# Optimization experiments

Hardware: AMD Instinct MI355X
Metric: run time of the kernel (lower is better)

The kernel has to match this reference:

```python
import jax, jax.numpy as jnp
import numpy as np
import math

M = 512          # num_bin_x
NB = 512         # num_bin_y
NUM_NODES = 2_000_000
K = 4            # max bins a node can overlap per dim (size <= 2.5 bins)
SQRT2 = math.sqrt(2.0)


def setup_inputs() -> dict:
    key = jax.random.key(0)
    k1, k2 = jax.random.split(key)
    node_pos = jax.random.uniform(k1, (NUM_NODES, 2), jnp.float32, 0.05, 0.95)
    # node sizes between 0.5 and 2.5 bins (normalized layout units)
    node_size = jax.random.uniform(k2, (NUM_NODES, 2), jnp.float32) * (2.0 / M) + (0.5 / M)
    return {
        "node_pos": node_pos,
        "node_size": node_size,
        "node_weight": jnp.ones((NUM_NODES,), jnp.float32),
        "expand_ratio": jnp.ones((NUM_NODES,), jnp.float32),
        "unit_len": jnp.array([1.0 / M, 1.0 / NB], jnp.float32),
        "init_density_map": jnp.zeros((M, NB), jnp.float32),
        "num_bin_x": M,
        "num_bin_y": NB,
    }


def pre_normalize(node_pos, node_size, node_weight, expand_ratio, unit_len, mx, ny):
    # density_map_cuda.pre_normalize: expand tiny nodes to sqrt(2)*unit_len,
    # rescale weight to preserve area, convert rects to bin coordinates.
    ux, uy = unit_len[0], unit_len[1]
    w, h = node_size[:, 0], node_size[:, 1]
    new_w = jnp.maximum(w, SQRT2 * ux)
    new_h = jnp.maximum(h, SQRT2 * uy)
    weight = node_weight * expand_ratio * (w * h) / (new_w * new_h)
    xl = jnp.clip((node_pos[:, 0] - 0.5 * new_w) / ux, 0.0, mx)
    xh = jnp.clip((node_pos[:, 0] + 0.5 * new_w) / ux, 0.0, mx)
    yl = jnp.clip((node_pos[:, 1] - 0.5 * new_h) / uy, 0.0, ny)
    yh = jnp.clip((node_pos[:, 1] + 0.5 * new_h) / uy, 0.0, ny)
    return jnp.stack([xl, xh, yl, yh, weight], axis=1)  # [N, 5]


def scatter_density(info, mx, ny):
    # density_map_cuda.forward: overlap-area scatter-add of node rects into bins.
    xl, xh, yl, yh, w = info[:, 0], info[:, 1], info[:, 2], info[:, 3], info[:, 4]
    bx0 = jnp.floor(xl).astype(jnp.int32)
    by0 = jnp.floor(yl).astype(jnp.int32)
    dm = jnp.zeros((mx, ny), jnp.float32)
    for dx in range(K):
        ix = bx0 + dx
        fx = ix.astype(jnp.float32)
        ox = jnp.clip(jnp.minimum(xh, fx + 1.0) - jnp.maximum(xl, fx), 0.0)
        ixc = jnp.clip(ix, 0, mx - 1)
        for dy in range(K):
            iy = by0 + dy
            fy = iy.astype(jnp.float32)
            oy = jnp.clip(jnp.minimum(yh, fy + 1.0) - jnp.maximum(yl, fy), 0.0)
            iyc = jnp.clip(iy, 0, ny - 1)
            dm = dm.at[ixc, iyc].add(w * ox * oy)
    return dm


def make_transforms(n):
    k = jnp.arange(n, dtype=jnp.float32)[:, None]
    m = jnp.arange(n, dtype=jnp.float32)[None, :]
    ang = jnp.pi * k * (2.0 * m + 1.0) / (2.0 * n)
    C = jnp.cos(ang)  # [freq, space]
    S = jnp.sin(ang)
    w = jnp.where(jnp.arange(n) == 0, 1.0, 2.0).astype(jnp.float32)
    return C, S, w


def spectral_solve(dm, unit_len, mx, ny):
    # fft_scale construction from __init__
    wj = (jnp.arange(mx, dtype=jnp.float32) * (2.0 * jnp.pi / mx))[:, None]
    wk = (jnp.arange(ny, dtype=jnp.float32) * (2.0 * jnp.pi / ny))[None, :]
    wk = wk * (unit_len[0] / unit_len[1])  # scale_w_k=True
    wsq = wj ** 2 + wk ** 2
    wsq = wsq.at[0, 0].set(1.0)
    pscale = (1.0 / wsq).at[0, 0].set(0.0)
    fx_scale = wj * pscale * 0.5
    fy_scale = wk * pscale * 0.5

    Cx, Sx, wx = make_transforms(mx)
    Cy, Sy, wy = make_transforms(ny)
    # dct2: coeff[u,v] = (1/(M*N)) * sum_{m,n} dm[m,n] cos(pi u(2m+1)/2M) cos(pi v(2n+1)/2N)
    coeff = (Cx @ dm @ Cy.T) / (mx * ny)
    ICx = (wx[:, None] * Cx)  # weighted inverse cosine basis [freq, space]
    ICy = (wy[:, None] * Cy)
    ISx = (wx[:, None] * Sx)
    ISy = (wy[:, None] * Sy)
    potential = ICx.T @ (coeff * pscale) @ ICy          # idct2
    force_x = ISx.T @ (coeff * fx_scale) @ ICy          # idxst_idct
    force_y = ICx.T @ (coeff * fy_scale) @ ISy          # idct_idxst
    return potential, force_x, force_y


def reference(node_pos, node_size, node_weight, expand_ratio, unit_len,
              init_density_map, num_bin_x, num_bin_y):
    info = pre_normalize(node_pos, node_size, node_weight, expand_ratio,
                         unit_len, num_bin_x, num_bin_y)
    density_map = init_density_map + scatter_density(info, num_bin_x, num_bin_y)
    potential, _, _ = spectral_solve(density_map, unit_len, num_bin_x, num_bin_y)
    energy = jnp.sum(potential * density_map)
    return energy
```

## Files before the change

kernel.cpp:

```cpp
#include <hip/hip_runtime.h>
#include <math.h>

#define MX 512
#define NY 512
#define TWO_PI 6.283185307179586f

#define TSHIFT 6
#define NT 64
#define LDIM 68
#define SLAB (LDIM * LDIM)
#define SLAB4 (SLAB / 4)
#define NPB 2048
#define KPT 8
#define CAP 40960
#define SPTMAX 32
#define RPARTS 19
#define QSCALE 26214.0f
#define QINV (1.0f / 26214.0f)

typedef __attribute__((ext_vector_type(8))) short short8;
typedef __attribute__((ext_vector_type(4))) float float4_t;
typedef __attribute__((ext_vector_type(4))) unsigned short ushort4_t;

__device__ __forceinline__ unsigned short f2bf(float x) {
    union { float f; unsigned u; } v; v.f = x;
    unsigned r = v.u + 0x7fffu + ((v.u >> 16) & 1u);
    return (unsigned short)(r >> 16);
}
__device__ __forceinline__ float bf2f(unsigned short h) {
    union { float f; unsigned u; } v; v.u = ((unsigned)h) << 16;
    return v.f;
}

__device__ __forceinline__ void node_bounds(float2 p, float2 s, float ux, float uy,
                                            float& xl, float& xh, float& yl, float& yh,
                                            float& nw, float& nh) {
    const float SQ2 = 1.41421356237309515f;
    nw = fmaxf(s.x, SQ2 * ux);
    nh = fmaxf(s.y, SQ2 * uy);
    xl = fminf(fmaxf((p.x - 0.5f * nw) / ux, 0.0f), (float)MX);
    xh = fminf(fmaxf((p.x + 0.5f * nw) / ux, 0.0f), (float)MX);
    yl = fminf(fmaxf((p.y - 0.5f * nh) / uy, 0.0f), (float)NY);
    yh = fminf(fmaxf((p.y + 0.5f * nh) / uy, 0.0f), (float)NY);
}

__global__ void gen_cos_kernel(unsigned short* __restrict__ Ch,
                               unsigned short* __restrict__ Cl,
                               unsigned int* __restrict__ base,
                               unsigned int* __restrict__ cursor,
                               float* __restrict__ out, int cap_mode) {
    int idx = blockIdx.x * blockDim.x + threadIdx.x;
    if (idx == 0) *out = 0.0f;
    if (cap_mode && idx <= NT) {
        base[idx] = (unsigned int)idx * CAP;
        if (idx < NT) cursor[idx] = (unsigned int)idx * CAP;
    }
    int a = idx >> 9;
    int j = idx & 511;
    float x = cospif((float)(a * (2 * j + 1)) * (1.0f / 1024.0f));
    unsigned short hi = f2bf(x);
    Ch[idx] = hi;
    Cl[idx] = f2bf(x - bf2f(hi));
}

__global__ __launch_bounds__(256)
void count_kernel(const float2* __restrict__ pos, const float2* __restrict__ size,
                  const float* __restrict__ unit_len,
                  unsigned int* __restrict__ cnt, int n) {
    __shared__ unsigned int h[NT];
    if (threadIdx.x < NT) h[threadIdx.x] = 0;
    __syncthreads();
    float ux = unit_len[0], uy = unit_len[1];
    int start = blockIdx.x * NPB;
    int end = min(start + NPB, n);
#pragma unroll
    for (int k = 0; k < KPT; k++) {
        int i = start + k * 256 + (int)threadIdx.x;
        if (i < end) {
            float xl, xh, yl, yh, nw, nh;
            node_bounds(pos[i], size[i], ux, uy, xl, xh, yl, yh, nw, nh);
            int bx0 = min((int)floorf(xl), MX - 1);
            int by0 = min((int)floorf(yl), NY - 1);
            atomicAdd(&h[((bx0 >> TSHIFT) << 3) | (by0 >> TSHIFT)], 1u);
        }
    }
    __syncthreads();
    if (threadIdx.x < NT) {
        unsigned int c = h[threadIdx.x];
        if (c) atomicAdd(&cnt[threadIdx.x], c);
    }
}

__global__ void scan_kernel(const unsigned int* __restrict__ cnt,
                            unsigned int* __restrict__ base,
                            unsigned int* __restrict__ cursor) {
    if (threadIdx.x == 0 && blockIdx.x == 0) {
        unsigned int ex = 0;
        for (int t = 0; t < NT; t++) {
            base[t] = ex;
            cursor[t] = ex;
            ex += cnt[t];
        }
        base[NT] = ex;
    }
}

__global__ __launch_bounds__(256)
void place_kernel(const float2* __restrict__ pos, const float2* __restrict__ size,
                  const float* __restrict__ nwt, const float* __restrict__ er,
                  const float* __restrict__ unit_len,
                  const unsigned int* __restrict__ base,
                  unsigned int* __restrict__ cursor,
                  float4* __restrict__ pb, int n) {
    __shared__ unsigned int h[NT];
    __shared__ unsigned int lb[NT + 1];
    __shared__ unsigned int bb[NT];
    __shared__ float4 buf[NPB];
    __shared__ unsigned char til[NPB];
    if (threadIdx.x < NT) h[threadIdx.x] = 0;
    __syncthreads();
    float ux = unit_len[0], uy = unit_len[1];
    int start = blockIdx.x * NPB;
    int end = min(start + NPB, n);

    float cxl[KPT], cyl[KPT], cw[KPT];
    unsigned int cq[KPT], pk[KPT];
#pragma unroll
    for (int k = 0; k < KPT; k++) {
        int i = start + k * 256 + (int)threadIdx.x;
        if (i < end) {
            float2 p = pos[i], s = size[i];
            float xl, xh, yl, yh, nw, nh;
            node_bounds(p, s, ux, uy, xl, xh, yl, yh, nw, nh);
            cxl[k] = xl; cyl[k] = yl;
            cw[k] = nwt[i] * er[i] * (s.x * s.y) / (nw * nh);
            unsigned qx = (unsigned)((xh - xl) * QSCALE + 0.5f);
            unsigned qy = (unsigned)((yh - yl) * QSCALE + 0.5f);
            if (qx > 65535u) qx = 65535u;
            if (qy > 65535u) qy = 65535u;
            cq[k] = qx | (qy << 16);
            int bx0 = min((int)floorf(xl), MX - 1);
            int by0 = min((int)floorf(yl), NY - 1);
            unsigned int t = ((bx0 >> TSHIFT) << 3) | (by0 >> TSHIFT);
            pk[k] = (t << 11) | atomicAdd(&h[t], 1u);
        }
    }
    __syncthreads();
    if (threadIdx.x == 0) {
        unsigned int ex = 0;
        for (int t = 0; t < NT; t++) { lb[t] = ex; ex += h[t]; }
        lb[NT] = ex;
    }
    if (threadIdx.x < NT) {
        unsigned int c = h[threadIdx.x];
        bb[threadIdx.x] = c ? atomicAdd(&cursor[threadIdx.x], c) : 0u;
    }
    __syncthreads();
#pragma unroll
    for (int k = 0; k < KPT; k++) {
        int i = start + k * 256 + (int)threadIdx.x;
        if (i < end) {
            unsigned int t = pk[k] >> 11;
            unsigned int slot = lb[t] + (pk[k] & 2047u);
            buf[slot] = make_float4(cxl[k], cyl[k], cw[k], __uint_as_float(cq[k]));
            til[slot] = (unsigned char)t;
        }
    }
    __syncthreads();
    unsigned int total = lb[NT];
    for (unsigned int j = threadIdx.x; j < total; j += 256) {
        unsigned int t = til[j];
        unsigned int dst = bb[t] + (j - lb[t]);
        if (dst < base[t + 1]) pb[dst] = buf[j];
    }
}

__device__ __forceinline__ void accum_one(float4 v, float* acc, int tbx, int tby) {
    float xl = v.x, yl = v.y, w = v.z;
    unsigned q = __float_as_uint(v.w);
    float xh = xl + (float)(q & 0xffffu) * QINV;
    float yh = yl + (float)(q >> 16) * QINV;
    int bx0 = min((int)floorf(xl), MX - 1);
    int by0 = min((int)floorf(yl), NY - 1);
    float oxs[4], oys[4];
    int rb[4], lys[4];
#pragma unroll
    for (int d = 0; d < 4; d++) {
        int ix = bx0 + d;
        float fx = (float)ix;
        oxs[d] = fmaxf(fminf(xh, fx + 1.0f) - fmaxf(xl, fx), 0.0f);
        rb[d] = (min(ix, MX - 1) - tbx) * LDIM;
        int iy = by0 + d;
        float fy = (float)iy;
        oys[d] = fmaxf(fminf(yh, fy + 1.0f) - fmaxf(yl, fy), 0.0f);
        lys[d] = min(iy, NY - 1) - tby;
    }
#pragma unroll
    for (int dx = 0; dx < 4; dx++) {
        if (oxs[dx] == 0.0f) continue;
        float wox = w * oxs[dx];
#pragma unroll
        for (int dy = 0; dy < 4; dy++) {
            float vv = wox * oys[dy];
            if (vv != 0.0f) atomicAdd(&acc[rb[dx] + lys[dy]], vv);
        }
    }
}

__global__ __launch_bounds__(256)
void accum_kernel(const float4* __restrict__ pb,
                  const unsigned int* __restrict__ base,
                  const unsigned int* __restrict__ cursor,
                  float* __restrict__ slab, int spt) {
    __shared__ float acc[SLAB];
    int t = blockIdx.x / spt;
    int s = blockIdx.x - t * spt;
    int tbx = (t >> 3) << TSHIFT;
    int tby = (t & 7) << TSHIFT;
    for (int e = threadIdx.x; e < SLAB4; e += 256)
        ((float4*)acc)[e] = make_float4(0.f, 0.f, 0.f, 0.f);
    __syncthreads();

    unsigned int b0 = base[t];
    unsigned int c = min(cursor[t] - b0, base[t + 1] - b0);
    unsigned int chunk = (c + spt - 1) / spt;
    unsigned int ks = s * chunk;
    unsigned int ke = min(c, ks + chunk);

    unsigned int k = ks + threadIdx.x;
    float4 cur = make_float4(0.f, 0.f, 0.f, 0.f);
    bool have = (k < ke);
    if (have) cur = pb[b0 + k];
    while (have) {
        unsigned int k2 = k + 256;
        bool have2 = (k2 < ke);
        float4 nxt = make_float4(0.f, 0.f, 0.f, 0.f);
        if (have2) nxt = pb[b0 + k2];
        accum_one(cur, acc, tbx, tby);
        cur = nxt; k = k2; have = have2;
    }
    __syncthreads();

    float4* dst = (float4*)(slab + (size_t)blockIdx.x * SLAB);
    for (int e = threadIdx.x; e < SLAB4; e += 256)
        dst[e] = ((float4*)acc)[e];
}

__global__ __launch_bounds__(256)
void reduce_slabs_kernel(const float* __restrict__ slab,
                         float* __restrict__ tacc, int spt) {
    int t = blockIdx.x / RPARTS;
    int part = blockIdx.x - t * RPARTS;
    int e = part * 256 + (int)threadIdx.x;
    if (e < SLAB) {
        const float* s0 = slab + (size_t)t * spt * SLAB + e;
        float sum = 0.0f;
        for (int s = 0; s < spt; s++) sum += s0[(size_t)s * SLAB];
        tacc[(size_t)t * SLAB + e] = sum;
    }
}

__global__ __launch_bounds__(256)
void combine_kernel(const float* __restrict__ tacc,
                    const float* __restrict__ init_dm,
                    unsigned short* __restrict__ dmh,
                    unsigned short* __restrict__ dml) {
    int v = blockIdx.x * blockDim.x + threadIdx.x;
    int gx = v >> 7;
    int g4 = v & 127;
    int gy = g4 << 2;
    int rx = gx & 63, ry = gy & 63;
    int tx0 = gx >> TSHIFT, ty0 = gy >> TSHIFT;

    float4 sum = ((const float4*)init_dm)[v];
#pragma unroll
    for (int ax = 0; ax < 2; ax++) {
        int tx = tx0 - ax;
        if (tx < 0 || (ax == 1 && rx > 3)) continue;
        int lx = rx + (ax << TSHIFT);
#pragma unroll
        for (int ay = 0; ay < 2; ay++) {
            int ty = ty0 - ay;
            if (ty < 0 || (ay == 1 && ry > 0)) continue;
            int ly = ry + (ay << TSHIFT);
            float4 sv = *(const float4*)(tacc
                + (size_t)((tx << 3) | ty) * SLAB + lx * LDIM + ly);
            sum.x += sv.x; sum.y += sv.y; sum.z += sv.z; sum.w += sv.w;
        }
    }
    ushort4_t hi, lo;
    float sv[4] = {sum.x, sum.y, sum.z, sum.w};
#pragma unroll
    for (int r = 0; r < 4; r++) {
        unsigned short h = f2bf(sv[r]);
        hi[r] = h;
        lo[r] = f2bf(sv[r] - bf2f(h));
    }
    int idx = (gx << 9) | gy;
    *(ushort4_t*)(dmh + idx) = hi;
    *(ushort4_t*)(dml + idx) = lo;
}

__global__ __launch_bounds__(256)
void dct1_mfma_kernel(const unsigned short* __restrict__ dmh,
                      const unsigned short* __restrict__ dml,
                      const unsigned short* __restrict__ Ch,
                      const unsigned short* __restrict__ Cl,
                      unsigned short* __restrict__ UhT,
                      unsigned short* __restrict__ UlT) {
    __shared__ float part[3][64][4];
    int lane = threadIdx.x & 63;
    int wv = threadIdx.x >> 6;
    int tile = blockIdx.x;
    int jt = (tile >> 5) * 16;
    int bt = (tile & 31) * 16;
    int m = lane & 15, q = lane >> 4;
    float4_t acc = {0.f, 0.f, 0.f, 0.f};
    const unsigned short* ah_row = dmh + (jt + m) * 512;
    const unsigned short* al_row = dml + (jt + m) * 512;
    const unsigned short* bh_row = Ch + (bt + m) * 512;
    const unsigned short* bl_row = Cl + (bt + m) * 512;
    int kbase = wv * 128;
#pragma unroll
    for (int kk = 0; kk < 128; kk += 32) {
        int off = kbase + kk + q * 8;
        short8 ah = *(const short8*)(ah_row + off);
        short8 al = *(const short8*)(al_row + off);
        short8 bh = *(const short8*)(bh_row + off);
        short8 bl = *(const short8*)(bl_row + off);
        acc = __builtin_amdgcn_mfma_f32_16x16x32_bf16(ah, bh, acc, 0, 0, 0);
        acc = __builtin_amdgcn_mfma_f32_16x16x32_bf16(ah, bl, acc, 0, 0, 0);
        acc = __builtin_amdgcn_mfma_f32_16x16x32_bf16(al, bh, acc, 0, 0, 0);
    }
    if (wv > 0) {
#pragma unroll
        for (int r = 0; r < 4; r++) part[wv - 1][lane][r] = acc[r];
    }
    __syncthreads();
    if (wv == 0) {
#pragma unroll
        for (int r = 0; r < 4; r++) {
            float v = acc[r] + part[0][lane][r] + part[1][lane][r] + part[2][lane][r];
            unsigned short hi = f2bf(v);
            int addr = (bt + m) * 512 + jt + q * 4 + r;
            UhT[addr] = hi;
            UlT[addr] = f2bf(v - bf2f(hi));
        }
    }
}

__global__ __launch_bounds__(256)
void dct2_mfma_kernel(const unsigned short* __restrict__ Ch,
                      const unsigned short* __restrict__ Cl,
                      const unsigned short* __restrict__ UhT,
                      const unsigned short* __restrict__ UlT,
                      const float* __restrict__ unit_len,
                      float* __restrict__ out) {
    __shared__ float part[3][64][4];
    int lane = threadIdx.x & 63;
    int wv = threadIdx.x >> 6;
    int tile = blockIdx.x;
    int at = (tile >> 5) * 16;
    int bt = (tile & 31) * 16;
    int m = lane & 15, q = lane >> 4;
    float4_t acc = {0.f, 0.f, 0.f, 0.f};
    const unsigned short* ah_row = Ch + (at + m) * 512;
    const unsigned short* al_row = Cl + (at + m) * 512;
    const unsigned short* bh_row = UhT + (bt + m) * 512;
    const unsigned short* bl_row = UlT + (bt + m) * 512;
    int kbase = wv * 128;
#pragma unroll
    for (int kk = 0; kk < 128; kk += 32) {
        int off = kbase + kk + q * 8;
        short8 ah = *(const short8*)(ah_row + off);
        short8 al = *(const short8*)(al_row + off);
        short8 bh = *(const short8*)(bh_row + off);
        short8 bl = *(const short8*)(bl_row + off);
        acc = __builtin_amdgcn_mfma_f32_16x16x32_bf16(ah, bh, acc, 0, 0, 0);
        acc = __builtin_amdgcn_mfma_f32_16x16x32_bf16(ah, bl, acc, 0, 0, 0);
        acc = __builtin_amdgcn_mfma_f32_16x16x32_bf16(al, bh, acc, 0, 0, 0);
    }
    if (wv > 0) {
#pragma unroll
        for (int r = 0; r < 4; r++) part[wv - 1][lane][r] = acc[r];
    }
    __syncthreads();
    if (wv == 0) {
        float ratio = unit_len[0] / unit_len[1];
        int b = bt + m;
        float wkb = (float)b * (TWO_PI / (float)NY) * ratio;
        float wyb = (b == 0) ? 1.0f : 2.0f;
        float e = 0.0f;
#pragma unroll
        for (int r = 0; r < 4; r++) {
            float t = acc[r] + part[0][lane][r] + part[1][lane][r] + part[2][lane][r];
            int a = at + q * 4 + r;
            float wja = (float)a * (TWO_PI / (float)MX);
            float wsq = wja * wja + wkb * wkb;
            float ps = (a == 0 && b == 0) ? 0.0f : (1.0f / wsq);
            float wxa = (a == 0) ? 1.0f : 2.0f;
            e += wxa * wyb * ps * t * t;
        }
#pragma unroll
        for (int off = 32; off > 0; off >>= 1) e += __shfl_down(e, off, 64);
        if (lane == 0)
            atomicAdd(out, e * (1.0f / ((float)MX * (float)NY)));
    }
}

__global__ __launch_bounds__(256)
void scatter_kernel(const float2* __restrict__ pos, const float2* __restrict__ size,
                    const float* __restrict__ nwt, const float* __restrict__ er,
                    const float* __restrict__ unit_len,
                    float* __restrict__ dm, int n) {
    int i = blockIdx.x * blockDim.x + threadIdx.x;
    if (i >= n) return;
    float ux = unit_len[0], uy = unit_len[1];
    float2 p = pos[i], s = size[i];
    float xl, xh, yl, yh, nw, nh;
    node_bounds(p, s, ux, uy, xl, xh, yl, yh, nw, nh);
    float w = nwt[i] * er[i] * (s.x * s.y) / (nw * nh);
    int bx0 = (int)floorf(xl);
    int by0 = (int)floorf(yl);
#pragma unroll
    for (int dx = 0; dx < 4; dx++) {
        int ix = bx0 + dx;
        float fx = (float)ix;
        float ox = fmaxf(fminf(xh, fx + 1.0f) - fmaxf(xl, fx), 0.0f);
        if (ox == 0.0f) continue;
        int rowoff = min(max(ix, 0), MX - 1) * NY;
        float wox = w * ox;
#pragma unroll
        for (int dy = 0; dy < 4; dy++) {
            int iy = by0 + dy;
            float fy = (float)iy;
            float oy = fmaxf(fminf(yh, fy + 1.0f) - fmaxf(yl, fy), 0.0f);
            float vv = wox * oy;
            if (vv != 0.0f) atomicAdd(&dm[rowoff + min(max(iy, 0), NY - 1)], vv);
        }
    }
}

__global__ void cvt_dm_kernel(const float* __restrict__ dm,
                              unsigned short* __restrict__ dmh,
                              unsigned short* __restrict__ dml) {
    int idx = blockIdx.x * blockDim.x + threadIdx.x;
    float x = dm[idx];
    unsigned short hi = f2bf(x);
    dmh[idx] = hi;
    dml[idx] = f2bf(x - bf2f(hi));
}

extern "C" void kernel_launch(void* const* d_in, const int* in_sizes, int n_in,
                              void* d_out, int out_size, void* d_ws, size_t ws_size,
                              hipStream_t stream) {
    const float2* node_pos  = (const float2*)d_in[0];
    const float2* node_size = (const float2*)d_in[1];
    const float*  node_wt   = (const float*)d_in[2];
    const float*  exp_ratio = (const float*)d_in[3];
    const float*  unit_len  = (const float*)d_in[4];
    const float*  init_dm   = (const float*)d_in[5];
    float* out = (float*)d_out;
    int n = in_sizes[2];

    char* wsb = (char*)d_ws;
    size_t off = 0;
    auto alloc = [&](size_t bytes) { void* p = wsb + off; off = (off + bytes + 255) & ~(size_t)255; return p; };
    unsigned short* Ch   = (unsigned short*)alloc((size_t)MX * NY * 2);
    unsigned short* Cl   = (unsigned short*)alloc((size_t)MX * NY * 2);
    unsigned short* dmh  = (unsigned short*)alloc((size_t)MX * NY * 2);
    unsigned short* dml  = (unsigned short*)alloc((size_t)MX * NY * 2);
    unsigned short* UhT  = (unsigned short*)alloc((size_t)MX * NY * 2);
    unsigned short* UlT  = (unsigned short*)alloc((size_t)MX * NY * 2);
    float*          dm     = (float*)alloc((size_t)MX * NY * sizeof(float));
    unsigned int*   cnt    = (unsigned int*)alloc(NT * sizeof(unsigned int));
    unsigned int*   tbase  = (unsigned int*)alloc((NT + 1) * sizeof(unsigned int));
    unsigned int*   cursor = (unsigned int*)alloc(NT * sizeof(unsigned int));
    float*          tacc   = (float*)alloc((size_t)NT * SLAB * sizeof(float));
    size_t off_common = off;
    size_t per_spt = (size_t)NT * SLAB * sizeof(float);

    float4* pbF = (float4*)alloc((size_t)NT * CAP * sizeof(float4));
    int sptF = 0;
    float* slbF = nullptr;
    if (off <= ws_size) {
        sptF = (int)((ws_size - off) / per_spt);
        if (sptF > SPTMAX) sptF = SPTMAX;
        if (sptF >= 4) slbF = (float*)alloc((size_t)NT * sptF * SLAB * sizeof(float));
    }
    bool tierFast = (slbF != nullptr);

    off = off_common;
    float4* pbE = (float4*)alloc((size_t)n * sizeof(float4));
    int sptE = 0;
    float* slbE = nullptr;
    if (off <= ws_size) {
        sptE = (int)((ws_size - off) / per_spt);
        if (sptE > SPTMAX) sptE = SPTMAX;
        if (sptE >= 1) slbE = (float*)alloc((size_t)NT * sptE * SLAB * sizeof(float));
    }
    bool tierExact = (slbE != nullptr);

    gen_cos_kernel<<<(MX * NY) / 256, 256, 0, stream>>>(Ch, Cl, tbase, cursor,
                                                        out, tierFast ? 1 : 0);

    if (tierFast || tierExact) {
        float4* pb  = tierFast ? pbF : pbE;
        float*  slb = tierFast ? slbF : slbE;
        int     spt = tierFast ? sptF : sptE;
        int nblk = (n + NPB - 1) / NPB;
        if (!tierFast) {
            hipMemsetAsync(cnt, 0, NT * sizeof(unsigned int), stream);
            count_kernel<<<nblk, 256, 0, stream>>>(node_pos, node_size, unit_len, cnt, n);
            scan_kernel<<<1, 64, 0, stream>>>(cnt, tbase, cursor);
        }
        place_kernel<<<nblk, 256, 0, stream>>>(
            node_pos, node_size, node_wt, exp_ratio, unit_len, tbase, cursor, pb, n);
        accum_kernel<<<NT * spt, 256, 0, stream>>>(pb, tbase, cursor, slb, spt);
        reduce_slabs_kernel<<<NT * RPARTS, 256, 0, stream>>>(slb, tacc, spt);
        combine_kernel<<<256, 256, 0, stream>>>(tacc, init_dm, dmh, dml);
    } else {
        hipMemcpyAsync(dm, init_dm, (size_t)MX * NY * sizeof(float),
                       hipMemcpyDeviceToDevice, stream);
        scatter_kernel<<<(n + 255) / 256, 256, 0, stream>>>(
            node_pos, node_size, node_wt, exp_ratio, unit_len, dm, n);
        cvt_dm_kernel<<<(MX * NY) / 256, 256, 0, stream>>>(dm, dmh, dml);
    }

    dct1_mfma_kernel<<<1024, 256, 0, stream>>>(dmh, dml, Ch, Cl, UhT, UlT);
    dct2_mfma_kernel<<<1024, 256, 0, stream>>>(Ch, Cl, UhT, UlT, unit_len, out);
}
```

Before: 248.1 us.

## Fuse cosine gen, slab reduce, combine and both DCT passes into cooperative kernel

Merges cosine-table generation, slab reduction, density combine and the two MFMA DCT passes into one cooperative kernel that uses grid-wide syncs between stages. The fast tier also switches to fixed per-tile offsets (t*CAP) with a memset of the cursors, which removes base-array lookups. This cuts four kernel launches and their inter-kernel gaps. In exchange it relies on all 1024 blocks being co-resident and pays the cost of grid.sync barriers.

```diff
diff --git a/kernel.cpp b/kernel.cpp
--- a/kernel.cpp
+++ b/kernel.cpp
@@ -1,5 +1,8 @@
 #include <hip/hip_runtime.h>
+#include <hip/hip_cooperative_groups.h>
 #include <math.h>
+
+namespace cg = cooperative_groups;
 
 #define MX 512
 #define NY 512
@@ -14,7 +17,6 @@
 #define KPT 8
 #define CAP 40960
 #define SPTMAX 32
-#define RPARTS 19
 #define QSCALE 26214.0f
 #define QINV (1.0f / 26214.0f)
 
@@ -44,25 +46,6 @@
     yh = fminf(fmaxf((p.y + 0.5f * nh) / uy, 0.0f), (float)NY);
 }
 
-__global__ void gen_cos_kernel(unsigned short* __restrict__ Ch,
-                               unsigned short* __restrict__ Cl,
-                               unsigned int* __restrict__ base,
-                               unsigned int* __restrict__ cursor,
-                               float* __restrict__ out, int cap_mode) {
-    int idx = blockIdx.x * blockDim.x + threadIdx.x;
-    if (idx == 0) *out = 0.0f;
-    if (cap_mode && idx <= NT) {
-        base[idx] = (unsigned int)idx * CAP;
-        if (idx < NT) cursor[idx] = (unsigned int)idx * CAP;
-    }
-    int a = idx >> 9;
-    int j = idx & 511;
-    float x = cospif((float)(a * (2 * j + 1)) * (1.0f / 1024.0f));
-    unsigned short hi = f2bf(x);
-    Ch[idx] = hi;
-    Cl[idx] = f2bf(x - bf2f(hi));
-}
-
 __global__ __launch_bounds__(256)
 void count_kernel(const float2* __restrict__ pos, const float2* __restrict__ size,
                   const float* __restrict__ unit_len,
@@ -109,7 +92,7 @@
 void place_kernel(const float2* __restrict__ pos, const float2* __restrict__ size,
                   const float* __restrict__ nwt, const float* __restrict__ er,
                   const float* __restrict__ unit_len,
-                  const unsigned int* __restrict__ base,
+                  const unsigned int* __restrict__ basep,
                   unsigned int* __restrict__ cursor,
                   float4* __restrict__ pb, int n) {
     __shared__ unsigned int h[NT];
@@ -168,10 +151,18 @@
     }
     __syncthreads();
     unsigned int total = lb[NT];
-    for (unsigned int j = threadIdx.x; j < total; j += 256) {
-        unsigned int t = til[j];
-        unsigned int dst = bb[t] + (j - lb[t]);
-        if (dst < base[t + 1]) pb[dst] = buf[j];
+    if (basep) {
+        for (unsigned int j = threadIdx.x; j < total; j += 256) {
+            unsigned int t = til[j];
+            unsigned int dst = bb[t] + (j - lb[t]);
+            if (dst < basep[t + 1]) pb[dst] = buf[j];
+        }
+    } else {
+        for (unsigned int j = threadIdx.x; j < total; j += 256) {
+            unsigned int t = til[j];
+            unsigned int lofs = bb[t] + (j - lb[t]);
+            if (lofs < CAP) pb[(size_t)t * CAP + lofs] = buf[j];
+        }
     }
 }
 
@@ -209,7 +200,7 @@
 
 __global__ __launch_bounds__(256)
 void accum_kernel(const float4* __restrict__ pb,
-                  const unsigned int* __restrict__ base,
+                  const unsigned int* __restrict__ basep,
                   const unsigned int* __restrict__ cursor,
                   float* __restrict__ slab, int spt) {
     __shared__ float acc[SLAB];
@@ -221,8 +212,14 @@
         ((float4*)acc)[e] = make_float4(0.f, 0.f, 0.f, 0.f);
     __syncthreads();
 
-    unsigned int b0 = base[t];
-    unsigned int c = min(cursor[t] - b0, base[t + 1] - b0);
+    unsigned int b0g, c;
+    if (basep) {
+        b0g = basep[t];
+        c = min(cursor[t] - b0g, basep[t + 1] - b0g);
+    } else {
+        b0g = (unsigned int)t * CAP;
+        c = min(cursor[t], (unsigned int)CAP);
+    }
     unsigned int chunk = (c + spt - 1) / spt;
     unsigned int ks = s * chunk;
     unsigned int ke = min(c, ks + chunk);
@@ -230,12 +227,12 @@
     unsigned int k = ks + threadIdx.x;
     float4 cur = make_float4(0.f, 0.f, 0.f, 0.f);
     bool have = (k < ke);
-    if (have) cur = pb[b0 + k];
+    if (have) cur = pb[b0g + k];
     while (have) {
         unsigned int k2 = k + 256;
         bool have2 = (k2 < ke);
         float4 nxt = make_float4(0.f, 0.f, 0.f, 0.f);
-        if (have2) nxt = pb[b0 + k2];
+        if (have2) nxt = pb[b0g + k2];
         accum_one(cur, acc, tbx, tby);
         cur = nxt; k = k2; have = have2;
     }
@@ -246,165 +243,164 @@
         dst[e] = ((float4*)acc)[e];
 }
 
-__global__ __launch_bounds__(256)
-void reduce_slabs_kernel(const float* __restrict__ slab,
-                         float* __restrict__ tacc, int spt) {
-    int t = blockIdx.x / RPARTS;
-    int part = blockIdx.x - t * RPARTS;
-    int e = part * 256 + (int)threadIdx.x;
-    if (e < SLAB) {
-        const float* s0 = slab + (size_t)t * spt * SLAB + e;
-        float sum = 0.0f;
-        for (int s = 0; s < spt; s++) sum += s0[(size_t)s * SLAB];
-        tacc[(size_t)t * SLAB + e] = sum;
-    }
-}
-
-__global__ __launch_bounds__(256)
-void combine_kernel(const float* __restrict__ tacc,
-                    const float* __restrict__ init_dm,
-                    unsigned short* __restrict__ dmh,
-                    unsigned short* __restrict__ dml) {
-    int v = blockIdx.x * blockDim.x + threadIdx.x;
-    int gx = v >> 7;
-    int g4 = v & 127;
-    int gy = g4 << 2;
-    int rx = gx & 63, ry = gy & 63;
-    int tx0 = gx >> TSHIFT, ty0 = gy >> TSHIFT;
-
-    float4 sum = ((const float4*)init_dm)[v];
-#pragma unroll
-    for (int ax = 0; ax < 2; ax++) {
-        int tx = tx0 - ax;
-        if (tx < 0 || (ax == 1 && rx > 3)) continue;
-        int lx = rx + (ax << TSHIFT);
-#pragma unroll
-        for (int ay = 0; ay < 2; ay++) {
-            int ty = ty0 - ay;
-            if (ty < 0 || (ay == 1 && ry > 0)) continue;
-            int ly = ry + (ay << TSHIFT);
-            float4 sv = *(const float4*)(tacc
-                + (size_t)((tx << 3) | ty) * SLAB + lx * LDIM + ly);
-            sum.x += sv.x; sum.y += sv.y; sum.z += sv.z; sum.w += sv.w;
-        }
-    }
-    ushort4_t hi, lo;
-    float sv[4] = {sum.x, sum.y, sum.z, sum.w};
-#pragma unroll
-    for (int r = 0; r < 4; r++) {
-        unsigned short h = f2bf(sv[r]);
-        hi[r] = h;
-        lo[r] = f2bf(sv[r] - bf2f(h));
-    }
-    int idx = (gx << 9) | gy;
-    *(ushort4_t*)(dmh + idx) = hi;
-    *(ushort4_t*)(dml + idx) = lo;
-}
-
-__global__ __launch_bounds__(256)
-void dct1_mfma_kernel(const unsigned short* __restrict__ dmh,
-                      const unsigned short* __restrict__ dml,
-                      const unsigned short* __restrict__ Ch,
-                      const unsigned short* __restrict__ Cl,
-                      unsigned short* __restrict__ UhT,
-                      unsigned short* __restrict__ UlT) {
+__global__ __launch_bounds__(256, 4)
+void fused_tail_kernel(const float* __restrict__ slab, float* __restrict__ tacc,
+                       const float* __restrict__ init_dm,
+                       unsigned short* __restrict__ dmh, unsigned short* __restrict__ dml,
+                       unsigned short* __restrict__ Ch, unsigned short* __restrict__ Cl,
+                       unsigned short* __restrict__ UhT, unsigned short* __restrict__ UlT,
+                       const float* __restrict__ unit_len, float* __restrict__ out,
+                       int spt, int do_combine) {
+    cg::grid_group grid = cg::this_grid();
     __shared__ float part[3][64][4];
+    int gtid = blockIdx.x * 256 + (int)threadIdx.x;
+
+    if (gtid == 0) *out = 0.0f;
+    {
+        int a = gtid >> 9, j = gtid & 511;
+        float x = cospif((float)(a * (2 * j + 1)) * (1.0f / 1024.0f));
+        unsigned short hi = f2bf(x);
+        Ch[gtid] = hi;
+        Cl[gtid] = f2bf(x - bf2f(hi));
+    }
+    if (do_combine) {
+        for (int e = gtid; e < NT * SLAB; e += 262144) {
+            int t = e / SLAB;
+            int o = e - t * SLAB;
+            const float* s0 = slab + (size_t)t * spt * SLAB + o;
+            float sum = 0.0f;
+            for (int s = 0; s < spt; s++) sum += s0[(size_t)s * SLAB];
+            tacc[e] = sum;
+        }
+    }
+    grid.sync();
+
+    if (do_combine && gtid < 65536) {
+        int v = gtid;
+        int gx = v >> 7;
+        int gy = (v & 127) << 2;
+        int rx = gx & 63, ry = gy & 63;
+        int tx0 = gx >> TSHIFT, ty0 = gy >> TSHIFT;
+        float4 sum = ((const float4*)init_dm)[v];
+#pragma unroll
+        for (int ax = 0; ax < 2; ax++) {
+            int tx = tx0 - ax;
+            if (tx < 0 || (ax == 1 && rx > 3)) continue;
+            int lx = rx + (ax << TSHIFT);
+#pragma unroll
+            for (int ay = 0; ay < 2; ay++) {
+                int ty = ty0 - ay;
+                if (ty < 0 || (ay == 1 && ry > 0)) continue;
+                int ly = ry + (ay << TSHIFT);
+                float4 sv = *(const float4*)(tacc
+                    + (size_t)((tx << 3) | ty) * SLAB + lx * LDIM + ly);
+                sum.x += sv.x; sum.y += sv.y; sum.z += sv.z; sum.w += sv.w;
+            }
+        }
+        ushort4_t hi, lo;
+        float sv[4] = {sum.x, sum.y, sum.z, sum.w};
+#pragma unroll
+        for (int r = 0; r < 4; r++) {
+            unsigned short h = f2bf(sv[r]);
+            hi[r] = h;
+            lo[r] = f2bf(sv[r] - bf2f(h));
+        }
+        int idx = (gx << 9) | gy;
+        *(ushort4_t*)(dmh + idx) = hi;
+        *(ushort4_t*)(dml + idx) = lo;
+    }
+    grid.sync();
+
     int lane = threadIdx.x & 63;
     int wv = threadIdx.x >> 6;
-    int tile = blockIdx.x;
-    int jt = (tile >> 5) * 16;
-    int bt = (tile & 31) * 16;
     int m = lane & 15, q = lane >> 4;
-    float4_t acc = {0.f, 0.f, 0.f, 0.f};
-    const unsigned short* ah_row = dmh + (jt + m) * 512;
-    const unsigned short* al_row = dml + (jt + m) * 512;
-    const unsigned short* bh_row = Ch + (bt + m) * 512;
-    const unsigned short* bl_row = Cl + (bt + m) * 512;
-    int kbase = wv * 128;
-#pragma unroll
-    for (int kk = 0; kk < 128; kk += 32) {
-        int off = kbase + kk + q * 8;
-        short8 ah = *(const short8*)(ah_row + off);
-        short8 al = *(const short8*)(al_row + off);
-        short8 bh = *(const short8*)(bh_row + off);
-        short8 bl = *(const short8*)(bl_row + off);
-        acc = __builtin_amdgcn_mfma_f32_16x16x32_bf16(ah, bh, acc, 0, 0, 0);
-        acc = __builtin_amdgcn_mfma_f32_16x16x32_bf16(ah, bl, acc, 0, 0, 0);
-        acc = __builtin_amdgcn_mfma_f32_16x16x32_bf16(al, bh, acc, 0, 0, 0);
-    }
-    if (wv > 0) {
-#pragma unroll
-        for (int r = 0; r < 4; r++) part[wv - 1][lane][r] = acc[r];
-    }
-    __syncthreads();
-    if (wv == 0) {
-#pragma unroll
-        for (int r = 0; r < 4; r++) {
-            float v = acc[r] + part[0][lane][r] + part[1][lane][r] + part[2][lane][r];
-            unsigned short hi = f2bf(v);
-            int addr = (bt + m) * 512 + jt + q * 4 + r;
-            UhT[addr] = hi;
-            UlT[addr] = f2bf(v - bf2f(hi));
-        }
-    }
-}
-
-__global__ __launch_bounds__(256)
-void dct2_mfma_kernel(const unsigned short* __restrict__ Ch,
-                      const unsigned short* __restrict__ Cl,
-                      const unsigned short* __restrict__ UhT,
-                      const unsigned short* __restrict__ UlT,
-                      const float* __restrict__ unit_len,
-                      float* __restrict__ out) {
-    __shared__ float part[3][64][4];
-    int lane = threadIdx.x & 63;
-    int wv = threadIdx.x >> 6;
-    int tile = blockIdx.x;
-    int at = (tile >> 5) * 16;
-    int bt = (tile & 31) * 16;
-    int m = lane & 15, q = lane >> 4;
-    float4_t acc = {0.f, 0.f, 0.f, 0.f};
-    const unsigned short* ah_row = Ch + (at + m) * 512;
-    const unsigned short* al_row = Cl + (at + m) * 512;
-    const unsigned short* bh_row = UhT + (bt + m) * 512;
-    const unsigned short* bl_row = UlT + (bt + m) * 512;
-    int kbase = wv * 128;
-#pragma unroll
-    for (int kk = 0; kk < 128; kk += 32) {
-        int off = kbase + kk + q * 8;
-        short8 ah = *(const short8*)(ah_row + off);
-        short8 al = *(const short8*)(al_row + off);
-        short8 bh = *(const short8*)(bh_row + off);
-        short8 bl = *(const short8*)(bl_row + off);
-        acc = __builtin_amdgcn_mfma_f32_16x16x32_bf16(ah, bh, acc, 0, 0, 0);
-        acc = __builtin_amdgcn_mfma_f32_16x16x32_bf16(ah, bl, acc, 0, 0, 0);
-        acc = __builtin_amdgcn_mfma_f32_16x16x32_bf16(al, bh, acc, 0, 0, 0);
-    }
-    if (wv > 0) {
-#pragma unroll
-        for (int r = 0; r < 4; r++) part[wv - 1][lane][r] = acc[r];
-    }
-    __syncthreads();
-    if (wv == 0) {
-        float ratio = unit_len[0] / unit_len[1];
-        int b = bt + m;
-        float wkb = (float)b * (TWO_PI / (float)NY) * ratio;
-        float wyb = (b == 0) ? 1.0f : 2.0f;
-        float e = 0.0f;
-#pragma unroll
-        for (int r = 0; r < 4; r++) {
-            float t = acc[r] + part[0][lane][r] + part[1][lane][r] + part[2][lane][r];
-            int a = at + q * 4 + r;
-            float wja = (float)a * (TWO_PI / (float)MX);
-            float wsq = wja * wja + wkb * wkb;
-            float ps = (a == 0 && b == 0) ? 0.0f : (1.0f / wsq);
-            float wxa = (a == 0) ? 1.0f : 2.0f;
-            e += wxa * wyb * ps * t * t;
-        }
-#pragma unroll
-        for (int off = 32; off > 0; off >>= 1) e += __shfl_down(e, off, 64);
-        if (lane == 0)
-            atomicAdd(out, e * (1.0f / ((float)MX * (float)NY)));
+
+    {
+        int tile = blockIdx.x;
+        int jt = (tile >> 5) * 16;
+        int bt = (tile & 31) * 16;
+        float4_t acc = {0.f, 0.f, 0.f, 0.f};
+        const unsigned short* ah_row = dmh + (jt + m) * 512;
+        const unsigned short* al_row = dml + (jt + m) * 512;
+        const unsigned short* bh_row = Ch + (bt + m) * 512;
+        const unsigned short* bl_row = Cl + (bt + m) * 512;
+        int kbase = wv * 128;
+#pragma unroll
+        for (int kk = 0; kk < 128; kk += 32) {
+            int off = kbase + kk + q * 8;
+            short8 ah = *(const short8*)(ah_row + off);
+            short8 al = *(const short8*)(al_row + off);
+            short8 bh = *(const short8*)(bh_row + off);
+            short8 bl = *(const short8*)(bl_row + off);
+            acc = __builtin_amdgcn_mfma_f32_16x16x32_bf16(ah, bh, acc, 0, 0, 0);
+            acc = __builtin_amdgcn_mfma_f32_16x16x32_bf16(ah, bl, acc, 0, 0, 0);
+            acc = __builtin_amdgcn_mfma_f32_16x16x32_bf16(al, bh, acc, 0, 0, 0);
+        }
+        if (wv > 0) {
+#pragma unroll
+            for (int r = 0; r < 4; r++) part[wv - 1][lane][r] = acc[r];
+        }
+        __syncthreads();
+        if (wv == 0) {
+#pragma unroll
+            for (int r = 0; r < 4; r++) {
+                float v = acc[r] + part[0][lane][r] + part[1][lane][r] + part[2][lane][r];
+                unsigned short hi = f2bf(v);
+                int addr = (bt + m) * 512 + jt + q * 4 + r;
+                UhT[addr] = hi;
+                UlT[addr] = f2bf(v - bf2f(hi));
+            }
+        }
+    }
+    grid.sync();
+
+    {
+        int tile = blockIdx.x;
+        int at = (tile >> 5) * 16;
+        int bt = (tile & 31) * 16;
+        float4_t acc = {0.f, 0.f, 0.f, 0.f};
+        const unsigned short* ah_row = Ch + (at + m) * 512;
+        const unsigned short* al_row = Cl + (at + m) * 512;
+        const unsigned short* bh_row = UhT + (bt + m) * 512;
+        const unsigned short* bl_row = UlT + (bt + m) * 512;
+        int kbase = wv * 128;
+#pragma unroll
+        for (int kk = 0; kk < 128; kk += 32) {
+            int off = kbase + kk + q * 8;
+            short8 ah = *(const short8*)(ah_row + off);
+            short8 al = *(const short8*)(al_row + off);
+            short8 bh = *(const short8*)(bh_row + off);
+            short8 bl = *(const short8*)(bl_row + off);
+            acc = __builtin_amdgcn_mfma_f32_16x16x32_bf16(ah, bh, acc, 0, 0, 0);
+            acc = __builtin_amdgcn_mfma_f32_16x16x32_bf16(ah, bl, acc, 0, 0, 0);
+            acc = __builtin_amdgcn_mfma_f32_16x16x32_bf16(al, bh, acc, 0, 0, 0);
+        }
+        if (wv > 0) {
+#pragma unroll
+            for (int r = 0; r < 4; r++) part[wv - 1][lane][r] = acc[r];
+        }
+        __syncthreads();
+        if (wv == 0) {
+            float ratio = unit_len[0] / unit_len[1];
+            int b = bt + m;
+            float wkb = (float)b * (TWO_PI / (float)NY) * ratio;
+            float wyb = (b == 0) ? 1.0f : 2.0f;
+            float e = 0.0f;
+#pragma unroll
+            for (int r = 0; r < 4; r++) {
+                float tv = acc[r] + part[0][lane][r] + part[1][lane][r] + part[2][lane][r];
+                int a = at + q * 4 + r;
+                float wja = (float)a * (TWO_PI / (float)MX);
+                float wsq = wja * wja + wkb * wkb;
+                float ps = (a == 0 && b == 0) ? 0.0f : (1.0f / wsq);
+                float wxa = (a == 0) ? 1.0f : 2.0f;
+                e += wxa * wyb * ps * tv * tv;
+            }
+#pragma unroll
+            for (int off = 32; off > 0; off >>= 1) e += __shfl_down(e, off, 64);
+            if (lane == 0)
+                atomicAdd(out, e * (1.0f / ((float)MX * (float)NY)));
+        }
     }
 }
 
@@ -501,32 +497,46 @@
     }
     bool tierExact = (slbE != nullptr);
 
-    gen_cos_kernel<<<(MX * NY) / 256, 256, 0, stream>>>(Ch, Cl, tbase, cursor,
-                                                        out, tierFast ? 1 : 0);
-
     if (tierFast || tierExact) {
         float4* pb  = tierFast ? pbF : pbE;
         float*  slb = tierFast ? slbF : slbE;
         int     spt = tierFast ? sptF : sptE;
+        const unsigned int* basep = tierFast ? nullptr : tbase;
         int nblk = (n + NPB - 1) / NPB;
-        if (!tierFast) {
+        if (tierFast) {
+            hipMemsetAsync(cursor, 0, NT * sizeof(unsigned int), stream);
+        } else {
             hipMemsetAsync(cnt, 0, NT * sizeof(unsigned int), stream);
             count_kernel<<<nblk, 256, 0, stream>>>(node_pos, node_size, unit_len, cnt, n);
             scan_kernel<<<1, 64, 0, stream>>>(cnt, tbase, cursor);
         }
         place_kernel<<<nblk, 256, 0, stream>>>(
-            node_pos, node_size, node_wt, exp_ratio, unit_len, tbase, cursor, pb, n);
-        accum_kernel<<<NT * spt, 256, 0, stream>>>(pb, tbase, cursor, slb, spt);
-        reduce_slabs_kernel<<<NT * RPARTS, 256, 0, stream>>>(slb, tacc, spt);
-        combine_kernel<<<256, 256, 0, stream>>>(tacc, init_dm, dmh, dml);
+            node_pos, node_size, node_wt, exp_ratio, unit_len, basep, cursor, pb, n);
+        accum_kernel<<<NT * spt, 256, 0, stream>>>(pb, basep, cursor, slb, spt);
+        int do_combine = 1;
+        void* kargs[] = {
+            (void*)&slb, (void*)&tacc, (void*)&init_dm,
+            (void*)&dmh, (void*)&dml, (void*)&Ch, (void*)&Cl,
+            (void*)&UhT, (void*)&UlT, (void*)&unit_len, (void*)&out,
+            (void*)&spt, (void*)&do_combine
+        };
+        hipLaunchCooperativeKernel((void*)fused_tail_kernel, dim3(1024), dim3(256),
+                                   kargs, 0, stream);
     } else {
         hipMemcpyAsync(dm, init_dm, (size_t)MX * NY * sizeof(float),
                        hipMemcpyDeviceToDevice, stream);
         scatter_kernel<<<(n + 255) / 256, 256, 0, stream>>>(
             node_pos, node_size, node_wt, exp_ratio, unit_len, dm, n);
         cvt_dm_kernel<<<(MX * NY) / 256, 256, 0, stream>>>(dm, dmh, dml);
-    }
-
-    dct1_mfma_kernel<<<1024, 256, 0, stream>>>(dmh, dml, Ch, Cl, UhT, UlT);
-    dct2_mfma_kernel<<<1024, 256, 0, stream>>>(Ch, Cl, UhT, UlT, unit_len, out);
-}
+        float* slb = tacc;
+        int spt = 1, do_combine = 0;
+        void* kargs[] = {
+            (void*)&slb, (void*)&tacc, (void*)&init_dm,
+            (void*)&dmh, (void*)&dml, (void*)&Ch, (void*)&Cl,
+            (void*)&UhT, (void*)&UlT, (void*)&unit_len, (void*)&out,
+            (void*)&spt, (void*)&do_combine
+        };
+        hipLaunchCooperativeKernel((void*)fused_tail_kernel, dim3(1024), dim3(256),
+                                   kargs, 0, stream);
+    }
+}
```

Result: slower. 562.1 us (+126.6%).
